# Performance work log

Hardware: AMD Instinct MI355X
Metric: run time of the kernel (lower is better)

Reference implementation:

```python
import jax, jax.numpy as jnp
import numpy as np

S, B, E, H = 2048, 4, 512, 8
HD = E // H


def setup_inputs() -> dict:
    key = jax.random.key(0)
    ks = jax.random.split(key, 5)
    scale = 1.0 / np.sqrt(E)
    return {
        "query": jax.random.normal(ks[0], (S, B, E), jnp.float32),
        "key": jax.random.normal(ks[1], (S, B, E), jnp.float32),
        "value": jax.random.normal(ks[2], (S, B, E), jnp.float32),
        "in_proj_weight": jax.random.normal(ks[3], (3 * E, E), jnp.float32) * scale,
        "in_proj_bias": jnp.zeros((3 * E,), jnp.float32),
        "out_proj_weight": jax.random.normal(ks[4], (E, E), jnp.float32) * scale,
        "out_proj_bias": jnp.zeros((E,), jnp.float32),
    }


def reference(query, key, value, in_proj_weight, in_proj_bias, out_proj_weight, out_proj_bias):
    tgt_len, bsz, embed_dim = query.shape
    src_len = key.shape[0]
    # Quirk of this module: first chunk (w_qk) projects BOTH q and k; third chunk projects v.
    w_qk = in_proj_weight[:embed_dim]
    w_v = in_proj_weight[2 * embed_dim:]
    b_qk = in_proj_bias[:embed_dim]
    b_v = in_proj_bias[2 * embed_dim:]
    q = query @ w_qk.T + b_qk          # [S, B, E]
    k = key @ w_qk.T + b_qk
    v = value @ w_v.T + b_v
    # (S, B, E) -> (B*H, S, HD)
    def split_heads(x, n):
        return x.reshape(n, bsz * H, HD).transpose(1, 0, 2)
    q = split_heads(q, tgt_len) / jnp.sqrt(jnp.asarray(HD, q.dtype))
    k = split_heads(k, src_len)
    v = split_heads(v, src_len)
    scores = jnp.einsum("bqd,bkd->bqk", q, k)          # [B*H, S, S] full score matrix
    attn = jax.nn.softmax(scores, axis=-1)
    out = jnp.einsum("bqk,bkd->bqd", attn, v)          # [B*H, S, HD]
    out = out.transpose(1, 0, 2).reshape(tgt_len * bsz, embed_dim)
    out = out @ out_proj_weight.T + out_proj_bias
    return out.reshape(tgt_len, bsz, embed_dim)
```

## Files before the change

kernel.cpp:

```cpp
#include <hip/hip_runtime.h>
#include <hip/hip_bf16.h>

typedef __attribute__((ext_vector_type(8))) short s16x8;
typedef __attribute__((ext_vector_type(4))) short s16x4;
typedef __attribute__((ext_vector_type(4))) float f32x4;
typedef __attribute__((ext_vector_type(4))) _Float16 f16x4;

#if __has_builtin(__builtin_amdgcn_mfma_f32_16x16x16bf16_1k)
#define PV_USE_BF16 1
#else
#define PV_USE_BF16 0
#endif

#if __has_builtin(__builtin_amdgcn_exp2f)
#define EXP2F(x) __builtin_amdgcn_exp2f(x)
#else
#define EXP2F(x) exp2f(x)
#endif

#define S_LEN 2048
#define EMB   512
#define MROWS 8192

__device__ __forceinline__ float bf2f(short x) {
    union { float f; unsigned u; } z; z.u = ((unsigned)(unsigned short)x) << 16; return z.f;
}
__device__ __forceinline__ short f2bf(float f) {
    union { float f; unsigned u; } z; z.f = f;
    unsigned r = z.u + 0x7FFF + ((z.u >> 16) & 1);
    return (short)(r >> 16);
}
__device__ __forceinline__ short f2bf_fast(float f) {
    union { float f; unsigned u; } z; z.f = f;
    return (short)((z.u + 0x8000u) >> 16);
}
__device__ __forceinline__ short f2v(float f) {
#if PV_USE_BF16
    return f2bf(f);
#else
    union { _Float16 h; short s; } u; u.h = (_Float16)f; return u.s;
#endif
}

template<int AF32, int BF32>
__device__ __forceinline__ void gemm_mainloop(const void* __restrict__ Ag,
                                              const void* __restrict__ Bg,
                                              short* sA, short* sB,
                                              f32x4 acc[2][4], int K)
{
    const int tid  = threadIdx.x;
    const int lane = tid & 63;
    const int wv   = tid >> 6;
    const int l15  = lane & 15, quad = lane >> 4;
    const int wm   = (wv >> 1) * 32, wn = (wv & 1) * 64;

    f32x4 afr[2], bfr[2];
    s16x8 ahr, bhr;

    auto loadT = [&](const void* G, int kt, f32x4* fr, s16x8& hr, int F32) {
        if (F32) {
#pragma unroll
            for (int p = 0; p < 2; ++p) {
                int c = tid + p * 512;
                fr[p] = *(const f32x4*)((const float*)G + (size_t)(c >> 3) * K + kt + (c & 7) * 4);
            }
        } else {
            hr = *(const s16x8*)((const short*)G + (size_t)(tid >> 2) * K + kt + (tid & 3) * 8);
        }
    };
    auto commitT = [&](short* s, f32x4* fr, s16x8& hr, int F32) {
        if (F32) {
#pragma unroll
            for (int p = 0; p < 2; ++p) {
                int c = tid + p * 512;
                s16x4 o4;
                o4[0] = f2bf_fast(fr[p][0]); o4[1] = f2bf_fast(fr[p][1]);
                o4[2] = f2bf_fast(fr[p][2]); o4[3] = f2bf_fast(fr[p][3]);
                *(s16x4*)(s + c * 4) = o4;
            }
        } else {
            *(s16x8*)(s + tid * 8) = hr;
        }
    };

    loadT(Ag, 0, afr, ahr, AF32);
    loadT(Bg, 0, bfr, bhr, BF32);
    commitT(sA, afr, ahr, AF32);
    commitT(sB, bfr, bhr, BF32);
    __syncthreads();

    for (int kt = 0; kt < K; kt += 32) {
        const int ktn = (kt + 32 < K) ? kt + 32 : 0;
        loadT(Ag, ktn, afr, ahr, AF32);
        loadT(Bg, ktn, bfr, bhr, BF32);

        s16x8 aF[2], bF[4];
#pragma unroll
        for (int i = 0; i < 2; ++i)
            aF[i] = *(const s16x8*)(sA + (wm + i * 16 + l15) * 32 + quad * 8);
#pragma unroll
        for (int j = 0; j < 4; ++j)
            bF[j] = *(const s16x8*)(sB + (wn + j * 16 + l15) * 32 + quad * 8);
#pragma unroll
        for (int i = 0; i < 2; ++i)
#pragma unroll
            for (int j = 0; j < 4; ++j)
                acc[i][j] = __builtin_amdgcn_mfma_f32_16x16x32_bf16(aF[i], bF[j], acc[i][j], 0, 0, 0);

        __syncthreads();
        commitT(sA, afr, ahr, AF32);
        commitT(sB, bfr, bhr, BF32);
        __syncthreads();
    }
}

__global__ __launch_bounds__(512, 4) void qkv_proj(const float* __restrict__ query,
                                                   const float* __restrict__ key,
                                                   const float* __restrict__ value,
                                                   const float* __restrict__ W,
                                                   const float* __restrict__ bias,
                                                   short* __restrict__ q,
                                                   short* __restrict__ k,
                                                   short* __restrict__ vt)
{
    __shared__ __align__(16) short sA[4096], sB[4096];
    const int z = blockIdx.z;
    const float* X  = (z == 0) ? query : (z == 1) ? key : value;
    const float* Wz = W    + (z == 2 ? (size_t)1024 * EMB : 0);
    const float* bz = bias + (z == 2 ? 1024 : 0);
    const float scale = (z == 0) ? 0.125f * 1.44269504f : 1.0f;

    const int blockM = blockIdx.x * 128, blockN = blockIdx.y * 128;

    f32x4 acc[2][4];
#pragma unroll
    for (int i = 0; i < 2; ++i)
#pragma unroll
        for (int j = 0; j < 4; ++j)
            acc[i][j] = (f32x4){0.f, 0.f, 0.f, 0.f};

    gemm_mainloop<1, 1>(X + (size_t)blockM * EMB, Wz + (size_t)blockN * EMB,
                        sA, sB, acc, EMB);

    const int tid = threadIdx.x, lane = tid & 63, wv = tid >> 6;
    const int l15 = lane & 15, quad = lane >> 4;
    const int wm = (wv >> 1) * 32, wn = (wv & 1) * 64;

#pragma unroll
    for (int j = 0; j < 4; ++j) {
        int col = blockN + wn + j * 16 + l15;
        float bval = bz[col];
        int h = col >> 6, hd = col & 63;
#pragma unroll
        for (int i = 0; i < 2; ++i) {
#pragma unroll
            for (int r = 0; r < 4; ++r) {
                int row = blockM + wm + i * 16 + quad * 4 + r;
                int s = row >> 2, b = row & 3;
                float val = (acc[i][j][r] + bval) * scale;
                int bh = b * 8 + h;
                if (z == 2) {
                    vt[((size_t)(bh * 64 + hd)) * 2048 + s] = f2v(val);
                } else {
                    short* dst = (z == 0) ? q : k;
                    dst[((size_t)(bh * 2048 + s)) * 64 + hd] = f2bf(val);
                }
            }
        }
    }
}

__global__ __launch_bounds__(256, 4) void flash_attn(const short* __restrict__ q,
                                                     const short* __restrict__ k,
                                                     const short* __restrict__ vt,
                                                     short* __restrict__ attn)
{
    __shared__ __align__(16) short sK[64 * 72];
    __shared__ __align__(16) short sV[64 * 72];
    const int bh = blockIdx.x;
    const int q0 = blockIdx.y * 64;
    const int tid = threadIdx.x, wv = tid >> 6, lane = tid & 63;
    const int l15 = lane & 15, quad = lane >> 4;

    const short* qp = q + ((size_t)(bh * 2048 + q0 + wv * 16 + l15)) * 64 + quad * 8;
    s16x8 qf0 = *(const s16x8*)qp;
    s16x8 qf1 = *(const s16x8*)(qp + 32);

    const short* kg = k  + (size_t)bh * 2048 * 64;
    const short* vg = vt + (size_t)bh * 64 * 2048;

    const int r0 = tid >> 3,          c0 = (tid & 7) * 8;
    const int r1 = (tid + 256) >> 3,  c1 = ((tid + 256) & 7) * 8;

#if PV_USE_BF16
    typedef s16x4 pvec;
#else
    typedef f16x4 pvec;
#endif

    f32x4 o[4];
    float lsum = 0.f;
#pragma unroll
    for (int i = 0; i < 4; ++i) o[i] = (f32x4){0.f, 0.f, 0.f, 0.f};

    s16x8 ka = *(const s16x8*)(kg + (size_t)r0 * 64 + c0);
    s16x8 kb = *(const s16x8*)(kg + (size_t)r1 * 64 + c1);
    s16x8 va = *(const s16x8*)(vg + (size_t)r0 * 2048 + c0);
    s16x8 vb = *(const s16x8*)(vg + (size_t)r1 * 2048 + c1);
    *(s16x8*)(sK + r0 * 72 + c0) = ka;
    *(s16x8*)(sK + r1 * 72 + c1) = kb;
    *(s16x8*)(sV + r0 * 72 + c0) = va;
    *(s16x8*)(sV + r1 * 72 + c1) = vb;
    __syncthreads();

    for (int kt = 0; kt < 2048; kt += 64) {
        const int ktn = (kt + 64) & 2047;
        ka = *(const s16x8*)(kg + (size_t)(ktn + r0) * 64 + c0);
        kb = *(const s16x8*)(kg + (size_t)(ktn + r1) * 64 + c1);
        va = *(const s16x8*)(vg + (size_t)r0 * 2048 + ktn + c0);
        vb = *(const s16x8*)(vg + (size_t)r1 * 2048 + ktn + c1);

        f32x4 sc[4];
#pragma unroll
        for (int ct = 0; ct < 4; ++ct) {
            s16x8 kf0 = *(const s16x8*)(sK + (ct * 16 + l15) * 72 + quad * 8);
            s16x8 kf1 = *(const s16x8*)(sK + (ct * 16 + l15) * 72 + quad * 8 + 32);
            f32x4 c = (f32x4){0.f, 0.f, 0.f, 0.f};
            c = __builtin_amdgcn_mfma_f32_16x16x32_bf16(kf0, qf0, c, 0, 0, 0);
            c = __builtin_amdgcn_mfma_f32_16x16x32_bf16(kf1, qf1, c, 0, 0, 0);
            sc[ct] = c;
        }
        pvec pf[4];
#pragma unroll
        for (int ct = 0; ct < 4; ++ct)
#pragma unroll
            for (int r = 0; r < 4; ++r) {
                float p = EXP2F(sc[ct][r]);
                lsum += p;
#if PV_USE_BF16
                pf[ct][r] = f2bf_fast(p);
#else
                pf[ct][r] = (_Float16)p;
#endif
            }
#pragma unroll
        for (int nt = 0; nt < 4; ++nt)
#pragma unroll
            for (int ct = 0; ct < 4; ++ct) {
                pvec vf = *(const pvec*)(sV + (nt * 16 + l15) * 72 + ct * 16 + quad * 4);
#if PV_USE_BF16
                o[nt] = __builtin_amdgcn_mfma_f32_16x16x16bf16_1k(pf[ct], vf, o[nt], 0, 0, 0);
#else
                o[nt] = __builtin_amdgcn_mfma_f32_16x16x16f16(pf[ct], vf, o[nt], 0, 0, 0);
#endif
            }
        __syncthreads();
        *(s16x8*)(sK + r0 * 72 + c0) = ka;
        *(s16x8*)(sK + r1 * 72 + c1) = kb;
        *(s16x8*)(sV + r0 * 72 + c0) = va;
        *(s16x8*)(sV + r1 * 72 + c1) = vb;
        __syncthreads();
    }

    float s = lsum;
    s += __shfl_xor(s, 16, 64);
    s += __shfl_xor(s, 32, 64);
    float sinv = 1.0f / s;
    float inv[4];
#pragma unroll
    for (int r = 0; r < 4; ++r)
        inv[r] = __shfl(sinv, quad * 20 + r, 64);

    const int b = bh >> 3, h = bh & 7;
#pragma unroll
    for (int r = 0; r < 4; ++r) {
        int srow = q0 + wv * 16 + quad * 4 + r;
#pragma unroll
        for (int nt = 0; nt < 4; ++nt)
            attn[(size_t)(srow * 4 + b) * 512 + h * 64 + nt * 16 + l15] = f2bf(o[nt][r] * inv[r]);
    }
}

__global__ __launch_bounds__(512, 4) void out_proj(const short* __restrict__ attn,
                                                   const float* __restrict__ W,
                                                   const float* __restrict__ bias,
                                                   float* __restrict__ out)
{
    __shared__ __align__(16) short sA[4096], sB[4096];
    const int blockM = blockIdx.x * 128, blockN = blockIdx.y * 128;

    f32x4 acc[2][4];
#pragma unroll
    for (int i = 0; i < 2; ++i)
#pragma unroll
        for (int j = 0; j < 4; ++j)
            acc[i][j] = (f32x4){0.f, 0.f, 0.f, 0.f};

    gemm_mainloop<0, 1>(attn + (size_t)blockM * EMB, W + (size_t)blockN * EMB,
                        sA, sB, acc, EMB);

    const int tid = threadIdx.x, lane = tid & 63, wv = tid >> 6;
    const int l15 = lane & 15, quad = lane >> 4;
    const int wm = (wv >> 1) * 32, wn = (wv & 1) * 64;

#pragma unroll
    for (int j = 0; j < 4; ++j) {
        int col = blockN + wn + j * 16 + l15;
        float bval = bias[col];
#pragma unroll
        for (int i = 0; i < 2; ++i) {
#pragma unroll
            for (int r = 0; r < 4; ++r) {
                int row = blockM + wm + i * 16 + quad * 4 + r;
                out[(size_t)row * 512 + col] = acc[i][j][r] + bval;
            }
        }
    }
}

extern "C" void kernel_launch(void* const* d_in, const int* in_sizes, int n_in,
                              void* d_out, int out_size, void* d_ws, size_t ws_size,
                              hipStream_t stream)
{
    const float* query = (const float*)d_in[0];
    const float* key   = (const float*)d_in[1];
    const float* value = (const float*)d_in[2];
    const float* ipw   = (const float*)d_in[3];
    const float* ipb   = (const float*)d_in[4];
    const float* opw   = (const float*)d_in[5];
    const float* opb   = (const float*)d_in[6];
    float* out = (float*)d_out;

    const size_t NELEM = (size_t)MROWS * EMB;
    short* q    = (short*)d_ws;
    short* k    = q + NELEM;
    short* attn = k + NELEM;
    short* vt   = (short*)d_out;

    qkv_proj  <<<dim3(64, 4, 3), 512, 0, stream>>>(query, key, value, ipw, ipb, q, k, vt);
    flash_attn<<<dim3(32, 32),   256, 0, stream>>>(q, k, vt, attn);
    out_proj  <<<dim3(64, 4),    512, 0, stream>>>(attn, opw, opb, out);
}
```

Measured before the change: 213.4 us.

## Double-buffer LDS tiles in GEMMs and attention, use 16x16x32 MFMA for PV

Shared-memory tiles in the GEMM mainloop and the flash attention loop become double-buffered. Each iteration writes the next tile into the alternate buffer and needs only one barrier instead of two. In attention, K rows are stored in a permuted order so the score layout matches a 16x16x32 bf16 MFMA operand, halving the PV MFMA count, and the row-sum accumulation is split into independent partials. This costs twice the LDS per block, which may reduce occupancy.

Measured after the change: 205.5 us. 3.7% less time.

```diff
diff --git a/kernel.cpp b/kernel.cpp
--- a/kernel.cpp
+++ b/kernel.cpp
@@ -4,13 +4,6 @@
 typedef __attribute__((ext_vector_type(8))) short s16x8;
 typedef __attribute__((ext_vector_type(4))) short s16x4;
 typedef __attribute__((ext_vector_type(4))) float f32x4;
-typedef __attribute__((ext_vector_type(4))) _Float16 f16x4;
-
-#if __has_builtin(__builtin_amdgcn_mfma_f32_16x16x16bf16_1k)
-#define PV_USE_BF16 1
-#else
-#define PV_USE_BF16 0
-#endif
 
 #if __has_builtin(__builtin_amdgcn_exp2f)
 #define EXP2F(x) __builtin_amdgcn_exp2f(x)
@@ -33,13 +26,6 @@
 __device__ __forceinline__ short f2bf_fast(float f) {
     union { float f; unsigned u; } z; z.f = f;
     return (short)((z.u + 0x8000u) >> 16);
-}
-__device__ __forceinline__ short f2v(float f) {
-#if PV_USE_BF16
-    return f2bf(f);
-#else
-    union { _Float16 h; short s; } u; u.h = (_Float16)f; return u.s;
-#endif
 }
 
 template<int AF32, int BF32>
@@ -89,28 +75,31 @@
     commitT(sB, bfr, bhr, BF32);
     __syncthreads();
 
+    int cur = 0;
     for (int kt = 0; kt < K; kt += 32) {
         const int ktn = (kt + 32 < K) ? kt + 32 : 0;
         loadT(Ag, ktn, afr, ahr, AF32);
         loadT(Bg, ktn, bfr, bhr, BF32);
 
+        const short* sAc = sA + cur * 4096;
+        const short* sBc = sB + cur * 4096;
         s16x8 aF[2], bF[4];
 #pragma unroll
         for (int i = 0; i < 2; ++i)
-            aF[i] = *(const s16x8*)(sA + (wm + i * 16 + l15) * 32 + quad * 8);
+            aF[i] = *(const s16x8*)(sAc + (wm + i * 16 + l15) * 32 + quad * 8);
 #pragma unroll
         for (int j = 0; j < 4; ++j)
-            bF[j] = *(const s16x8*)(sB + (wn + j * 16 + l15) * 32 + quad * 8);
+            bF[j] = *(const s16x8*)(sBc + (wn + j * 16 + l15) * 32 + quad * 8);
 #pragma unroll
         for (int i = 0; i < 2; ++i)
 #pragma unroll
             for (int j = 0; j < 4; ++j)
                 acc[i][j] = __builtin_amdgcn_mfma_f32_16x16x32_bf16(aF[i], bF[j], acc[i][j], 0, 0, 0);
 
+        commitT(sA + (cur ^ 1) * 4096, afr, ahr, AF32);
+        commitT(sB + (cur ^ 1) * 4096, bfr, bhr, BF32);
         __syncthreads();
-        commitT(sA, afr, ahr, AF32);
-        commitT(sB, bfr, bhr, BF32);
-        __syncthreads();
+        cur ^= 1;
     }
 }
 
@@ -123,7 +112,7 @@
                                                    short* __restrict__ k,
                                                    short* __restrict__ vt)
 {
-    __shared__ __align__(16) short sA[4096], sB[4096];
+    __shared__ __align__(16) short sA[2 * 4096], sB[2 * 4096];
     const int z = blockIdx.z;
     const float* X  = (z == 0) ? query : (z == 1) ? key : value;
     const float* Wz = W    + (z == 2 ? (size_t)1024 * EMB : 0);
@@ -160,7 +149,7 @@
                 float val = (acc[i][j][r] + bval) * scale;
                 int bh = b * 8 + h;
                 if (z == 2) {
-                    vt[((size_t)(bh * 64 + hd)) * 2048 + s] = f2v(val);
+                    vt[((size_t)(bh * 64 + hd)) * 2048 + s] = f2bf(val);
                 } else {
                     short* dst = (z == 0) ? q : k;
                     dst[((size_t)(bh * 2048 + s)) * 64 + hd] = f2bf(val);
@@ -175,8 +164,8 @@
                                                      const short* __restrict__ vt,
                                                      short* __restrict__ attn)
 {
-    __shared__ __align__(16) short sK[64 * 72];
-    __shared__ __align__(16) short sV[64 * 72];
+    __shared__ __align__(16) short sK[2][64 * 72];
+    __shared__ __align__(16) short sV[2][64 * 72];
     const int bh = blockIdx.x;
     const int q0 = blockIdx.y * 64;
     const int tid = threadIdx.x, wv = tid >> 6, lane = tid & 63;
@@ -191,28 +180,25 @@
 
     const int r0 = tid >> 3,          c0 = (tid & 7) * 8;
     const int r1 = (tid + 256) >> 3,  c1 = ((tid + 256) & 7) * 8;
-
-#if PV_USE_BF16
-    typedef s16x4 pvec;
-#else
-    typedef f16x4 pvec;
-#endif
+    const int p0 = (r0 & 35) | ((r0 & 24) >> 1) | ((r0 & 4) << 2);
+    const int p1 = (r1 & 35) | ((r1 & 24) >> 1) | ((r1 & 4) << 2);
 
     f32x4 o[4];
-    float lsum = 0.f;
-#pragma unroll
-    for (int i = 0; i < 4; ++i) o[i] = (f32x4){0.f, 0.f, 0.f, 0.f};
+    float ls[4];
+#pragma unroll
+    for (int i = 0; i < 4; ++i) { o[i] = (f32x4){0.f, 0.f, 0.f, 0.f}; ls[i] = 0.f; }
 
     s16x8 ka = *(const s16x8*)(kg + (size_t)r0 * 64 + c0);
     s16x8 kb = *(const s16x8*)(kg + (size_t)r1 * 64 + c1);
     s16x8 va = *(const s16x8*)(vg + (size_t)r0 * 2048 + c0);
     s16x8 vb = *(const s16x8*)(vg + (size_t)r1 * 2048 + c1);
-    *(s16x8*)(sK + r0 * 72 + c0) = ka;
-    *(s16x8*)(sK + r1 * 72 + c1) = kb;
-    *(s16x8*)(sV + r0 * 72 + c0) = va;
-    *(s16x8*)(sV + r1 * 72 + c1) = vb;
+    *(s16x8*)(sK[0] + p0 * 72 + c0) = ka;
+    *(s16x8*)(sK[0] + p1 * 72 + c1) = kb;
+    *(s16x8*)(sV[0] + r0 * 72 + c0) = va;
+    *(s16x8*)(sV[0] + r1 * 72 + c1) = vb;
     __syncthreads();
 
+    int cur = 0;
     for (int kt = 0; kt < 2048; kt += 64) {
         const int ktn = (kt + 64) & 2047;
         ka = *(const s16x8*)(kg + (size_t)(ktn + r0) * 64 + c0);
@@ -220,49 +206,48 @@
         va = *(const s16x8*)(vg + (size_t)r0 * 2048 + ktn + c0);
         vb = *(const s16x8*)(vg + (size_t)r1 * 2048 + ktn + c1);
 
+        const short* Kc = sK[cur];
+        const short* Vc = sV[cur];
+
         f32x4 sc[4];
 #pragma unroll
         for (int ct = 0; ct < 4; ++ct) {
-            s16x8 kf0 = *(const s16x8*)(sK + (ct * 16 + l15) * 72 + quad * 8);
-            s16x8 kf1 = *(const s16x8*)(sK + (ct * 16 + l15) * 72 + quad * 8 + 32);
+            s16x8 kf0 = *(const s16x8*)(Kc + (ct * 16 + l15) * 72 + quad * 8);
+            s16x8 kf1 = *(const s16x8*)(Kc + (ct * 16 + l15) * 72 + quad * 8 + 32);
             f32x4 c = (f32x4){0.f, 0.f, 0.f, 0.f};
             c = __builtin_amdgcn_mfma_f32_16x16x32_bf16(kf0, qf0, c, 0, 0, 0);
             c = __builtin_amdgcn_mfma_f32_16x16x32_bf16(kf1, qf1, c, 0, 0, 0);
             sc[ct] = c;
         }
-        pvec pf[4];
-#pragma unroll
-        for (int ct = 0; ct < 4; ++ct)
-#pragma unroll
-            for (int r = 0; r < 4; ++r) {
-                float p = EXP2F(sc[ct][r]);
-                lsum += p;
-#if PV_USE_BF16
-                pf[ct][r] = f2bf_fast(p);
-#else
-                pf[ct][r] = (_Float16)p;
-#endif
-            }
+        s16x8 pf[2];
+#pragma unroll
+        for (int c = 0; c < 2; ++c)
+#pragma unroll
+            for (int h = 0; h < 2; ++h)
+#pragma unroll
+                for (int r = 0; r < 4; ++r) {
+                    float p = EXP2F(sc[2 * c + h][r]);
+                    ls[r] += p;
+                    pf[c][h * 4 + r] = f2bf_fast(p);
+                }
 #pragma unroll
         for (int nt = 0; nt < 4; ++nt)
 #pragma unroll
-            for (int ct = 0; ct < 4; ++ct) {
-                pvec vf = *(const pvec*)(sV + (nt * 16 + l15) * 72 + ct * 16 + quad * 4);
-#if PV_USE_BF16
-                o[nt] = __builtin_amdgcn_mfma_f32_16x16x16bf16_1k(pf[ct], vf, o[nt], 0, 0, 0);
-#else
-                o[nt] = __builtin_amdgcn_mfma_f32_16x16x16f16(pf[ct], vf, o[nt], 0, 0, 0);
-#endif
-            }
+            for (int c = 0; c < 2; ++c) {
+                s16x8 vf = *(const s16x8*)(Vc + (nt * 16 + l15) * 72 + c * 32 + quad * 8);
+                o[nt] = __builtin_amdgcn_mfma_f32_16x16x32_bf16(pf[c], vf, o[nt], 0, 0, 0);
+            }
+        short* Kn = sK[cur ^ 1];
+        short* Vn = sV[cur ^ 1];
+        *(s16x8*)(Kn + p0 * 72 + c0) = ka;
+        *(s16x8*)(Kn + p1 * 72 + c1) = kb;
+        *(s16x8*)(Vn + r0 * 72 + c0) = va;
+        *(s16x8*)(Vn + r1 * 72 + c1) = vb;
         __syncthreads();
-        *(s16x8*)(sK + r0 * 72 + c0) = ka;
-        *(s16x8*)(sK + r1 * 72 + c1) = kb;
-        *(s16x8*)(sV + r0 * 72 + c0) = va;
-        *(s16x8*)(sV + r1 * 72 + c1) = vb;
-        __syncthreads();
-    }
-
-    float s = lsum;
+        cur ^= 1;
+    }
+
+    float s = ls[0] + ls[1] + ls[2] + ls[3];
     s += __shfl_xor(s, 16, 64);
     s += __shfl_xor(s, 32, 64);
     float sinv = 1.0f / s;
@@ -286,7 +271,7 @@
                                                    const float* __restrict__ bias,
                                                    float* __restrict__ out)
 {
-    __shared__ __align__(16) short sA[4096], sB[4096];
+    __shared__ __align__(16) short sA[2 * 4096], sB[2 * 4096];
     const int blockM = blockIdx.x * 128, blockN = blockIdx.y * 128;
 
     f32x4 acc[2][4];
```
